# Kernel tuning notes

Measured on AMD Instinct MI355X. Metric: run time of the kernel, lower is better.

## Reference

```python
import jax, jax.numpy as jnp
import numpy as np

_N_NEURONS = 16
_SCALE = 2.0 ** _N_NEURONS  # 65536, fixed-point quantization levels
_EPS = 1e-5


def _mtn(a, v_max):
    # fast multi-threshold neuron quantizer: floor to 2^-16 * v_max grid, saturate.
    a = jnp.maximum(a, 0.0)
    q = jnp.floor(a / v_max * _SCALE) / _SCALE * v_max
    q = jnp.minimum(q, v_max * (1.0 - 2.0 ** (-_N_NEURONS)))
    return jax.lax.stop_gradient(q)  # torch: i_out.detach()


def _oatn(x):
    # OATN fast / hight_acc / hight_acc_fast path, single predicated pass.
    xf = x.astype(jnp.float32)
    xc = jnp.clip(xf, -500.0, 500.0)
    signs = jax.lax.stop_gradient(jnp.sign(xc))
    a = jnp.abs(xc)
    # |x| < 10 -> quantize with v_max=10; |x| >= 10 -> v_max=500
    q = jnp.where(a < 10.0, _mtn(a, 10.0), _mtn(a, 500.0))
    return (q * signs).astype(x.dtype)


def setup_inputs() -> dict:
    key = jax.random.key(0)
    k1, k2, k3 = jax.random.split(key, 3)
    B, S, D = 4, 4096, 4096
    # scale so both quantization branches (|x|<10 and |x|>=10) are populated
    x = jax.random.normal(k1, (B, S, D), dtype=jnp.float32) * 8.0
    weight = 1.0 + 0.02 * jax.random.normal(k2, (D,), dtype=jnp.float32)
    bias = 0.02 * jax.random.normal(k3, (D,), dtype=jnp.float32)
    return {"x": x, "weight": weight, "bias": bias}


def reference(x, weight, bias):
    # spikeLN: spike-quantize activations, then LayerNorm over last dim.
    s = _oatn(x)                                   # [B, S, D]
    mu = jnp.mean(s, axis=-1, keepdims=True)       # [B, S, 1]
    var = jnp.mean((s - mu) ** 2, axis=-1, keepdims=True)
    y = (s - mu) * jax.lax.rsqrt(var + _EPS)
    return y * weight + bias
```

## Files before the change

kernel.cpp:

```cpp
#include <hip/hip_runtime.h>
#include <math.h>


#define LN_D      4096
#define LN_BLOCK  256

#define SAT10  ((float)(10.0  * (1.0 - 1.0/65536.0)))
#define SAT500 ((float)(500.0 * (1.0 - 1.0/65536.0)))

__device__ __forceinline__ float oatn_f32(float xf) {
    float xc = fminf(fmaxf(xf, -500.0f), 500.0f);
    float a  = fabsf(xc);
    bool small = (a < 10.0f);
    float vmax = small ? 10.0f  : 500.0f;
    float sat  = small ? SAT10  : SAT500;
    float q = floorf(a / vmax * 65536.0f) * (1.0f / 65536.0f) * vmax;
    q = fminf(q, sat);
    return copysignf(q, xc);
}

__global__ __launch_bounds__(LN_BLOCK, 4)
void spikeln_kernel(const float* __restrict__ x,
                    const float* __restrict__ w,
                    const float* __restrict__ b,
                    float* __restrict__ out)
{
    const int row = blockIdx.x;
    const size_t base = (size_t)row * LN_D;
    const float4* __restrict__ x4 = reinterpret_cast<const float4*>(x + base);
    float4* __restrict__ y4       = reinterpret_cast<float4*>(out + base);
    const float4* __restrict__ w4 = reinterpret_cast<const float4*>(w);
    const float4* __restrict__ b4 = reinterpret_cast<const float4*>(b);

    const int tid  = threadIdx.x;
    const int lane = tid & 63;
    const int wid  = tid >> 6;

    float s[16];
    float psum = 0.0f;

    #pragma unroll
    for (int c = 0; c < 4; ++c) {
        float4 v = x4[tid + c * LN_BLOCK];
        float q0 = oatn_f32(v.x);
        float q1 = oatn_f32(v.y);
        float q2 = oatn_f32(v.z);
        float q3 = oatn_f32(v.w);
        s[c * 4 + 0] = q0;
        s[c * 4 + 1] = q1;
        s[c * 4 + 2] = q2;
        s[c * 4 + 3] = q3;
        psum += (q0 + q1) + (q2 + q3);
    }

    __shared__ float red[8];

    float t = psum;
    #pragma unroll
    for (int off = 32; off > 0; off >>= 1) t += __shfl_down(t, off);
    if (lane == 0) red[wid] = t;
    __syncthreads();
    const float mu = (red[0] + red[1] + red[2] + red[3]) * (1.0f / (float)LN_D);

    float p2 = 0.0f;
    #pragma unroll
    for (int i = 0; i < 16; ++i) {
        float d = s[i] - mu;
        p2 += d * d;
    }
    t = p2;
    #pragma unroll
    for (int off = 32; off > 0; off >>= 1) t += __shfl_down(t, off);
    if (lane == 0) red[4 + wid] = t;
    __syncthreads();
    const float var = (red[4] + red[5] + red[6] + red[7]) * (1.0f / (float)LN_D);
    const float rstd = 1.0f / sqrtf(var + 1e-5f);

    #pragma unroll
    for (int c = 0; c < 4; ++c) {
        const int idx = tid + c * LN_BLOCK;
        float4 wv = w4[idx];
        float4 bv = b4[idx];
        float4 o;
        o.x = (s[c * 4 + 0] - mu) * rstd * wv.x + bv.x;
        o.y = (s[c * 4 + 1] - mu) * rstd * wv.y + bv.y;
        o.z = (s[c * 4 + 2] - mu) * rstd * wv.z + bv.z;
        o.w = (s[c * 4 + 3] - mu) * rstd * wv.w + bv.w;
        y4[idx] = o;
    }
}

extern "C" void kernel_launch(void* const* d_in, const int* in_sizes, int n_in,
                              void* d_out, int out_size, void* d_ws, size_t ws_size,
                              hipStream_t stream) {
    const float* x = (const float*)d_in[0];
    const float* w = (const float*)d_in[1];
    const float* b = (const float*)d_in[2];
    float* out = (float*)d_out;

    const int nrows = in_sizes[0] / LN_D;
    spikeln_kernel<<<nrows, LN_BLOCK, 0, stream>>>(x, w, b, out);
}
```

Measured before the change: 101.1 us.

## Use single-pass sum/sumsq stats, reciprocal quantizer, and nontemporal loads/stores

Computes mean and variance in a single reduction pass (sum and sum of squares with xor shuffles), which removes one block barrier and one reduction round. Replaces the division in the quantizer with multiplication by a precomputed reciprocal, and uses nontemporal loads and stores for the streamed input and output. The E[x^2]-mu^2 variance can lose precision, and the reciprocal multiply can shift floor boundaries slightly compared with the reference.

```diff
diff --git a/kernel.cpp b/kernel.cpp
--- a/kernel.cpp
+++ b/kernel.cpp
@@ -4,6 +4,8 @@
 
 #define LN_D      4096
 #define LN_BLOCK  256
+
+typedef float f32x4 __attribute__((ext_vector_type(4)));
 
 #define SAT10  ((float)(10.0  * (1.0 - 1.0/65536.0)))
 #define SAT500 ((float)(500.0 * (1.0 - 1.0/65536.0)))
@@ -12,9 +14,10 @@
     float xc = fminf(fmaxf(xf, -500.0f), 500.0f);
     float a  = fabsf(xc);
     bool small = (a < 10.0f);
-    float vmax = small ? 10.0f  : 500.0f;
-    float sat  = small ? SAT10  : SAT500;
-    float q = floorf(a / vmax * 65536.0f) * (1.0f / 65536.0f) * vmax;
+    float mul   = small ? (65536.0f / 10.0f) : (65536.0f / 500.0f);
+    float scale = small ? (10.0f / 65536.0f) : (500.0f / 65536.0f);
+    float sat   = small ? SAT10 : SAT500;
+    float q = floorf(a * mul) * scale;
     q = fminf(q, sat);
     return copysignf(q, xc);
 }
@@ -27,10 +30,10 @@
 {
     const int row = blockIdx.x;
     const size_t base = (size_t)row * LN_D;
-    const float4* __restrict__ x4 = reinterpret_cast<const float4*>(x + base);
-    float4* __restrict__ y4       = reinterpret_cast<float4*>(out + base);
-    const float4* __restrict__ w4 = reinterpret_cast<const float4*>(w);
-    const float4* __restrict__ b4 = reinterpret_cast<const float4*>(b);
+    const f32x4* __restrict__ x4 = reinterpret_cast<const f32x4*>(x + base);
+    f32x4* __restrict__ y4       = reinterpret_cast<f32x4*>(out + base);
+    const f32x4* __restrict__ w4 = reinterpret_cast<const f32x4*>(w);
+    const f32x4* __restrict__ b4 = reinterpret_cast<const f32x4*>(b);
 
     const int tid  = threadIdx.x;
     const int lane = tid & 63;
@@ -38,10 +41,11 @@
 
     float s[16];
     float psum = 0.0f;
+    float psq  = 0.0f;
 
     #pragma unroll
     for (int c = 0; c < 4; ++c) {
-        float4 v = x4[tid + c * LN_BLOCK];
+        f32x4 v = __builtin_nontemporal_load(&x4[tid + c * LN_BLOCK]);
         float q0 = oatn_f32(v.x);
         float q1 = oatn_f32(v.y);
         float q2 = oatn_f32(v.z);
@@ -51,42 +55,39 @@
         s[c * 4 + 2] = q2;
         s[c * 4 + 3] = q3;
         psum += (q0 + q1) + (q2 + q3);
+        psq = fmaf(q0, q0, psq);
+        psq = fmaf(q1, q1, psq);
+        psq = fmaf(q2, q2, psq);
+        psq = fmaf(q3, q3, psq);
     }
 
     __shared__ float red[8];
+    #pragma unroll
+    for (int off = 32; off > 0; off >>= 1) {
+        psum += __shfl_xor(psum, off);
+        psq  += __shfl_xor(psq,  off);
+    }
+    if (lane == 0) { red[wid] = psum; red[4 + wid] = psq; }
+    __syncthreads();
 
-    float t = psum;
-    #pragma unroll
-    for (int off = 32; off > 0; off >>= 1) t += __shfl_down(t, off);
-    if (lane == 0) red[wid] = t;
-    __syncthreads();
-    const float mu = (red[0] + red[1] + red[2] + red[3]) * (1.0f / (float)LN_D);
-
-    float p2 = 0.0f;
-    #pragma unroll
-    for (int i = 0; i < 16; ++i) {
-        float d = s[i] - mu;
-        p2 += d * d;
-    }
-    t = p2;
-    #pragma unroll
-    for (int off = 32; off > 0; off >>= 1) t += __shfl_down(t, off);
-    if (lane == 0) red[4 + wid] = t;
-    __syncthreads();
-    const float var = (red[4] + red[5] + red[6] + red[7]) * (1.0f / (float)LN_D);
+    const float sum = (red[0] + red[1]) + (red[2] + red[3]);
+    const float sq  = (red[4] + red[5]) + (red[6] + red[7]);
+    const float mu  = sum * (1.0f / (float)LN_D);
+    float var = sq * (1.0f / (float)LN_D) - mu * mu;
+    var = fmaxf(var, 0.0f);
     const float rstd = 1.0f / sqrtf(var + 1e-5f);
 
     #pragma unroll
     for (int c = 0; c < 4; ++c) {
         const int idx = tid + c * LN_BLOCK;
-        float4 wv = w4[idx];
-        float4 bv = b4[idx];
-        float4 o;
-        o.x = (s[c * 4 + 0] - mu) * rstd * wv.x + bv.x;
-        o.y = (s[c * 4 + 1] - mu) * rstd * wv.y + bv.y;
-        o.z = (s[c * 4 + 2] - mu) * rstd * wv.z + bv.z;
-        o.w = (s[c * 4 + 3] - mu) * rstd * wv.w + bv.w;
-        y4[idx] = o;
+        f32x4 wv = w4[idx];
+        f32x4 bv = b4[idx];
+        f32x4 o;
+        o.x = ((s[c * 4 + 0] - mu) * rstd) * wv.x + bv.x;
+        o.y = ((s[c * 4 + 1] - mu) * rstd) * wv.y + bv.y;
+        o.z = ((s[c * 4 + 2] - mu) * rstd) * wv.z + bv.z;
+        o.w = ((s[c * 4 + 3] - mu) * rstd) * wv.w + bv.w;
+        __builtin_nontemporal_store(o, &y4[idx]);
     }
 }
 
```

Measured after the change: 92.15 us. 8.9% less time.
